# Optimization experiments

Measured on AMD Instinct MI355X. Metric: run time of the kernel, lower is better.

Reference implementation:

```python
import jax, jax.numpy as jnp
import numpy as np

B, S = 512, 200            # batch, max_seq_len
D = H = 512                # embedding_dim must equal hidden_dim (ht init from embedded input)
VOCAB, USERS, SKILLS, OUT = 2002, 10000, 1001, 1001


def setup_inputs() -> dict:
    key = jax.random.key(0)
    ks = jax.random.split(key, 15)
    s = 0.05
    enc_emb = jax.random.normal(ks[0], (VOCAB, D)) * s
    enc_emb = enc_emb.at[0].set(0.0)  # padding_idx=0
    P = jax.random.normal(ks[1], (USERS, H)) * s
    Q = jax.random.normal(ks[2], (SKILLS, H)) * s
    P_bias = jax.random.normal(ks[3], (USERS, 1)) * s
    Q_bias = jax.random.normal(ks[4], (SKILLS, 1)) * s
    W_ih = jax.random.normal(ks[5], (4 * H, D)) * s   # torch LSTMCell weight_ih
    W_hh = jax.random.normal(ks[6], (4 * H, H)) * s   # torch LSTMCell weight_hh
    b_ih = jax.random.normal(ks[7], (4 * H,)) * s
    b_hh = jax.random.normal(ks[8], (4 * H,)) * s
    dec_W = jax.random.normal(ks[9], (OUT, H)) * s    # nn.Linear weight
    dec_b = jax.random.normal(ks[10], (OUT,)) * s
    main_input = jax.random.randint(ks[11], (B, S), 0, VOCAB)
    target_id = jax.random.randint(ks[12], (B, 1), 0, OUT)
    user_id_sequence = jax.random.randint(ks[13], (B, S), 0, USERS)
    skill_id_sequence = jax.random.randint(ks[14], (B, S), 0, SKILLS)
    return dict(main_input=main_input, target_id=target_id,
                user_id_sequence=user_id_sequence, skill_id_sequence=skill_id_sequence,
                enc_emb=enc_emb, P=P, Q=Q, P_bias=P_bias, Q_bias=Q_bias,
                W_ih=W_ih, W_hh=W_hh, b_ih=b_ih, b_hh=b_hh, dec_W=dec_W, dec_b=dec_b)


def reference(main_input, target_id, user_id_sequence, skill_id_sequence,
              enc_emb, P, Q, P_bias, Q_bias, W_ih, W_hh, b_ih, b_hh, dec_W, dec_b):
    x = enc_emb[main_input]                                    # [B,S,D] (dropout in eval mode = identity)
    # MF extended input: sigmoid(sum(P*Q, dim=2, keepdim) + P_bias + Q_bias) -> [B,S,1]
    mf = jax.nn.sigmoid(jnp.sum(P[user_id_sequence] * Q[skill_id_sequence], axis=2, keepdims=True)
                        + P_bias[user_id_sequence] + Q_bias[skill_id_sequence])

    def step(carry, inp):
        ht, ct = carry
        xt, et = inp                                           # xt:[B,D], et:[B,1]
        ct = ct + ct * et                                      # custom gating before cell update
        gates = xt @ W_ih.T + b_ih + ht @ W_hh.T + b_hh        # [B,4H], torch gate order i,f,g,o
        i, f, g, o = jnp.split(gates, 4, axis=-1)
        ct = jax.nn.sigmoid(f) * ct + jax.nn.sigmoid(i) * jnp.tanh(g)
        ht = jax.nn.sigmoid(o) * jnp.tanh(ct)
        return (ht, ct), None

    h0 = jnp.zeros((x.shape[0], H), x.dtype)
    (ht, _), _ = jax.lax.scan(step, (h0, h0),
                              (jnp.swapaxes(x, 0, 1), jnp.swapaxes(mf, 0, 1)))
    out = ht @ dec_W.T + dec_b                                 # [B,OUT]
    out = jnp.take_along_axis(out, target_id, axis=-1)         # [B,1]
    return jax.nn.sigmoid(out)
```

## Files before the change

### kernel.cpp

```cpp
#include <hip/hip_runtime.h>

typedef __attribute__((ext_vector_type(8))) short short8;
typedef __attribute__((ext_vector_type(4))) float floatx4;
typedef unsigned int uint;
typedef unsigned short ushort;
typedef unsigned long long ull;

#define B_ 512
#define S_ 200
#define H_ 512
#define VOCAB_ 2002

__device__ __forceinline__ ushort f2bfbits(float f) {
  union { float f; uint u; } c; c.f = f;
  uint u = c.u;
  u += 0x7fffu + ((u >> 16) & 1u);
  return (ushort)(u >> 16);
}
__device__ __forceinline__ float bf2f_(ushort u) {
  union { uint i; float f; } c; c.i = ((uint)u) << 16; return c.f;
}
__device__ __forceinline__ float sigmoidf_(float x) { return 1.f / (1.f + __expf(-x)); }
__device__ __forceinline__ float tanhf_(float x) { return 2.f / (1.f + __expf(-2.f * x)) - 1.f; }
__device__ __forceinline__ float clamp30(float x) { return fminf(fmaxf(x, -30.f), 30.f); }

__device__ __forceinline__ void split8(const float* p, short8& hi, short8& lo) {
#pragma unroll
  for (int j = 0; j < 8; ++j) {
    const float f = p[j];
    const ushort h = f2bfbits(f);
    hi[j] = (short)h;
    lo[j] = (short)f2bfbits(f - bf2f_(h));
  }
}

template <typename ET>
__global__ void encg_kernel(const float* __restrict__ emb, const float* __restrict__ Wih,
                            ET* __restrict__ encg) {
  const int w = threadIdx.x >> 6, l = threadIdx.x & 63;
  const int ln = l & 15, lk = l >> 4;
  const int n = (blockIdx.x * 4 + w) * 16 + ln;
  const int m = blockIdx.y * 16 + ln;
  const int mA = (m < VOCAB_) ? m : 0;
  const float* ap = emb + (size_t)mA * 512 + lk * 8;
  const float* bp = Wih + (size_t)n * 512 + lk * 8;
  floatx4 acc = {0.f, 0.f, 0.f, 0.f};
#pragma unroll 4
  for (int kk = 0; kk < 16; ++kk) {
    short8 ah, al, bh, bl;
    split8(ap + kk * 32, ah, al);
    split8(bp + kk * 32, bh, bl);
    acc = __builtin_amdgcn_mfma_f32_16x16x32_bf16(ah, bh, acc, 0, 0, 0);
    acc = __builtin_amdgcn_mfma_f32_16x16x32_bf16(ah, bl, acc, 0, 0, 0);
    acc = __builtin_amdgcn_mfma_f32_16x16x32_bf16(al, bh, acc, 0, 0, 0);
  }
#pragma unroll
  for (int r = 0; r < 4; ++r) {
    const int mo = blockIdx.y * 16 + lk * 4 + r;
    if (mo < VOCAB_) {
      if constexpr (sizeof(ET) == 2)
        encg[(size_t)mo * 2048 + n] = (ET)f2bfbits(acc[r]);
      else
        encg[(size_t)mo * 2048 + n] = acc[r];
    }
  }
}

__global__ void mf_kernel(const int* __restrict__ us, const int* __restrict__ ss,
                          const float* __restrict__ P, const float* __restrict__ Q,
                          const float* __restrict__ Pb, const float* __restrict__ Qb,
                          float* __restrict__ etb) {
  const int s = blockIdx.x;
  const int w = threadIdx.x >> 6, l = threadIdx.x & 63;
  const int b = blockIdx.y * 4 + w;
  const int u = us[b * S_ + s];
  const int k = ss[b * S_ + s];
  const float4 p0 = *(const float4*)(P + (size_t)u * 512 + l * 8);
  const float4 p1 = *(const float4*)(P + (size_t)u * 512 + l * 8 + 4);
  const float4 q0 = *(const float4*)(Q + (size_t)k * 512 + l * 8);
  const float4 q1 = *(const float4*)(Q + (size_t)k * 512 + l * 8 + 4);
  float dot = p0.x*q0.x + p0.y*q0.y + p0.z*q0.z + p0.w*q0.w
            + p1.x*q1.x + p1.y*q1.y + p1.z*q1.z + p1.w*q1.w;
#pragma unroll
  for (int off = 32; off > 0; off >>= 1) dot += __shfl_xor(dot, off);
  if (l == 0)
    etb[s * B_ + b] = sigmoidf_(dot + Pb[u] + Qb[k]);
}

template <typename ET>
__global__ __launch_bounds__(512, 2) void lstm_kernel(
    const int* __restrict__ tok, const ET* __restrict__ encg,
    const float* __restrict__ etb, const float* __restrict__ Whh,
    const float* __restrict__ bih, const float* __restrict__ bhh,
    ushort* ht_hi, ushort* ht_lo, int* ctr) {
  __shared__ __align__(16) ushort Ah_lds[32 * 528];
  __shared__ __align__(16) ushort Al_lds[32 * 528];
  __shared__ __align__(16) float gp_lds[128 * 36];

  const int bid = blockIdx.x;
  const int g = bid & 15, ns = bid >> 4;
  const int b0 = g * 32, h0 = ns * 32;
  const int tid = threadIdx.x;
  const int w = tid >> 6, l = tid & 63;
  const int ln = l & 15, lk = l >> 4;
  const int q = w >> 1;
  const int c0 = (w & 1) * 16;

  int* const myslot = ctr + g * 256 + ns * 16;
  int* const gslots = ctr + g * 256;

  short8 Bh[16], Bl[16];
  {
    const float* wr = Whh + (size_t)(q * 512 + h0 + c0 + ln) * 512 + lk * 8;
#pragma unroll 4
    for (int kk = 0; kk < 16; ++kk)
      split8(wr + kk * 32, Bh[kk], Bl[kk]);
  }

  const int sr = tid >> 4;
  const int sc = tid & 15;
  const int hh = sc * 2;
  const int bg = b0 + sr;
  float ct0 = 0.f, ct1 = 0.f;

  float bs[4][2];
#pragma unroll
  for (int qq = 0; qq < 4; ++qq) {
    const int col = qq * 512 + h0 + hh;
    bs[qq][0] = bih[col] + bhh[col];
    bs[qq][1] = bih[col + 1] + bhh[col + 1];
  }

  for (int s = 0; s < S_; ++s) {
    const int tv = tok[bg * S_ + s];
    float ev = etb[s * B_ + bg];
    float ex[4], ey[4];
#pragma unroll
    for (int qq = 0; qq < 4; ++qq) {
      if constexpr (sizeof(ET) == 2) {
        const uint e2 = *(const uint*)((const ushort*)encg + (size_t)tv * 2048 + qq * 512 + h0 + hh);
        ex[qq] = bf2f_((ushort)(e2 & 0xffffu)); ey[qq] = bf2f_((ushort)(e2 >> 16));
      } else {
        const float2 e = *(const float2*)((const float*)encg + (size_t)tv * 2048 + qq * 512 + h0 + hh);
        ex[qq] = e.x; ey[qq] = e.y;
      }
    }

    if (s > 0) {
      if (tid < 16) {
        while (__hip_atomic_load(gslots + tid * 16, __ATOMIC_RELAXED,
                                 __HIP_MEMORY_SCOPE_AGENT) < s) {}
      }
      __syncthreads();
    }
    const size_t rdo = (size_t)(s & 1) * (B_ * H_);
    const size_t wro = (size_t)((s & 1) ^ 1) * (B_ * H_);

    {
      const size_t go = rdo + (size_t)(b0 + sr) * 512 + sc * 32;
      const int lo_ = sr * 528 + sc * 32;
#pragma unroll
      for (int i = 0; i < 8; ++i)
        *(ull*)(Ah_lds + lo_ + i * 4) =
            __hip_atomic_load((const ull*)(ht_hi + go + i * 4), __ATOMIC_RELAXED, __HIP_MEMORY_SCOPE_AGENT);
#pragma unroll
      for (int i = 0; i < 8; ++i)
        *(ull*)(Al_lds + lo_ + i * 4) =
            __hip_atomic_load((const ull*)(ht_lo + go + i * 4), __ATOMIC_RELAXED, __HIP_MEMORY_SCOPE_AGENT);
    }
    __syncthreads();

    floatx4 acc[2];
    acc[0] = (floatx4){0.f, 0.f, 0.f, 0.f};
    acc[1] = (floatx4){0.f, 0.f, 0.f, 0.f};
#pragma unroll
    for (int mt = 0; mt < 2; ++mt)
#pragma unroll
      for (int kk = 0; kk < 16; ++kk) {
        const int ao = (mt * 16 + ln) * 528 + kk * 32 + lk * 8;
        const short8 ah = *(const short8*)(Ah_lds + ao);
        const short8 al = *(const short8*)(Al_lds + ao);
        acc[mt] = __builtin_amdgcn_mfma_f32_16x16x32_bf16(ah, Bh[kk], acc[mt], 0, 0, 0);
        acc[mt] = __builtin_amdgcn_mfma_f32_16x16x32_bf16(ah, Bl[kk], acc[mt], 0, 0, 0);
        acc[mt] = __builtin_amdgcn_mfma_f32_16x16x32_bf16(al, Bh[kk], acc[mt], 0, 0, 0);
      }
#pragma unroll
    for (int mt = 0; mt < 2; ++mt)
      *(floatx4*)(gp_lds + (w * 16 + ln) * 36 + mt * 16 + lk * 4) = acc[mt];
    __syncthreads();

    {
      ev = fminf(fmaxf(ev, 0.f), 1.f);
      float Gv[4][2];
#pragma unroll
      for (int qq = 0; qq < 4; ++qq) {
        Gv[qq][0] = clamp30(gp_lds[(qq * 32 + hh) * 36 + sr] + ex[qq] + bs[qq][0]);
        Gv[qq][1] = clamp30(gp_lds[(qq * 32 + hh + 1) * 36 + sr] + ey[qq] + bs[qq][1]);
      }
      const float scale = 1.f + ev;
      float c0v = ct0 * scale;
      c0v = sigmoidf_(Gv[1][0]) * c0v + sigmoidf_(Gv[0][0]) * tanhf_(Gv[2][0]);
      const float h0v = sigmoidf_(Gv[3][0]) * tanhf_(c0v);
      ct0 = c0v;
      float c1v = ct1 * scale;
      c1v = sigmoidf_(Gv[1][1]) * c1v + sigmoidf_(Gv[0][1]) * tanhf_(Gv[2][1]);
      const float h1v = sigmoidf_(Gv[3][1]) * tanhf_(c1v);
      ct1 = c1v;
      const ushort h0h = f2bfbits(h0v), h1h = f2bfbits(h1v);
      const ushort h0l = f2bfbits(h0v - bf2f_(h0h)), h1l = f2bfbits(h1v - bf2f_(h1h));
      const size_t wo = wro + (size_t)bg * 512 + h0 + hh;
      __hip_atomic_store((uint*)(ht_hi + wo), (uint)h0h | ((uint)h1h << 16),
                         __ATOMIC_RELAXED, __HIP_MEMORY_SCOPE_AGENT);
      __hip_atomic_store((uint*)(ht_lo + wo), (uint)h0l | ((uint)h1l << 16),
                         __ATOMIC_RELAXED, __HIP_MEMORY_SCOPE_AGENT);
    }
    __syncthreads();
    if (tid == 0)
      __hip_atomic_store(myslot, s + 1, __ATOMIC_RELAXED, __HIP_MEMORY_SCOPE_AGENT);
  }
}

__global__ void dec_kernel(const ushort* __restrict__ hthi, const ushort* __restrict__ htlo,
                           const float* __restrict__ decW, const float* __restrict__ decb,
                           const int* __restrict__ tgt, float* __restrict__ out) {
  const int w = threadIdx.x >> 6, l = threadIdx.x & 63;
  const int b = blockIdx.x * 4 + w;
  const int t = tgt[b];
  const uint4 hv = *(const uint4*)(hthi + (size_t)b * 512 + l * 8);
  const uint4 lv = *(const uint4*)(htlo + (size_t)b * 512 + l * 8);
  const float4 w0 = *(const float4*)(decW + (size_t)t * 512 + l * 8);
  const float4 w1 = *(const float4*)(decW + (size_t)t * 512 + l * 8 + 4);
  const uint ha[4] = {hv.x, hv.y, hv.z, hv.w};
  const uint la[4] = {lv.x, lv.y, lv.z, lv.w};
  float hf[8];
#pragma unroll
  for (int i = 0; i < 4; ++i) {
    hf[2*i]   = bf2f_((ushort)(ha[i] & 0xffffu)) + bf2f_((ushort)(la[i] & 0xffffu));
    hf[2*i+1] = bf2f_((ushort)(ha[i] >> 16))     + bf2f_((ushort)(la[i] >> 16));
  }
  float dot = hf[0]*w0.x + hf[1]*w0.y + hf[2]*w0.z + hf[3]*w0.w
            + hf[4]*w1.x + hf[5]*w1.y + hf[6]*w1.z + hf[7]*w1.w;
#pragma unroll
  for (int off = 32; off > 0; off >>= 1) dot += __shfl_xor(dot, off);
  if (l == 0) out[b] = sigmoidf_(dot + decb[t]);
}

extern "C" void kernel_launch(void* const* d_in, const int* in_sizes, int n_in,
                              void* d_out, int out_size, void* d_ws, size_t ws_size,
                              hipStream_t stream) {
  (void)in_sizes; (void)n_in; (void)out_size;
  const int* main_input = (const int*)d_in[0];
  const int* target_id  = (const int*)d_in[1];
  const int* user_seq   = (const int*)d_in[2];
  const int* skill_seq  = (const int*)d_in[3];
  const float* enc_emb  = (const float*)d_in[4];
  const float* P        = (const float*)d_in[5];
  const float* Q        = (const float*)d_in[6];
  const float* Pb       = (const float*)d_in[7];
  const float* Qb       = (const float*)d_in[8];
  const float* W_ih     = (const float*)d_in[9];
  const float* W_hh     = (const float*)d_in[10];
  const float* b_ih     = (const float*)d_in[11];
  const float* b_hh     = (const float*)d_in[12];
  const float* dec_W    = (const float*)d_in[13];
  const float* dec_b    = (const float*)d_in[14];
  float* out = (float*)d_out;

  char* wsb = (char*)d_ws;
  ushort* ht_hi = (ushort*)wsb;
  ushort* ht_lo = (ushort*)(wsb + 1048576);
  int* ctr = (int*)(wsb + 2097152);
  float* etb = (float*)(wsb + 2113536);
  char* encb = wsb + 2523136;
  const bool enc32 = ws_size >= (size_t)2523136 + 16400384;

  hipMemsetAsync(wsb, 0, 2113536, stream);

  if (enc32)
    encg_kernel<float><<<dim3(32, 126), dim3(256), 0, stream>>>(enc_emb, W_ih, (float*)encb);
  else
    encg_kernel<ushort><<<dim3(32, 126), dim3(256), 0, stream>>>(enc_emb, W_ih, (ushort*)encb);
  mf_kernel<<<dim3(200, 128), dim3(256), 0, stream>>>(user_seq, skill_seq, P, Q, Pb, Qb, etb);
  if (enc32)
    lstm_kernel<float><<<dim3(256), dim3(512), 0, stream>>>(
        main_input, (const float*)encb, etb, W_hh, b_ih, b_hh, ht_hi, ht_lo, ctr);
  else
    lstm_kernel<ushort><<<dim3(256), dim3(512), 0, stream>>>(
        main_input, (const ushort*)encb, etb, W_hh, b_ih, b_hh, ht_hi, ht_lo, ctr);
  dec_kernel<<<dim3(128), dim3(256), 0, stream>>>(ht_hi, ht_lo, dec_W, dec_b, target_id, out);
}
```

Before: 2.988 ms.

## Per-wave completion flags, split h-load pipelining, and XOR-swizzled LDS in LSTM step

Each wave now publishes its own progress flag after waiting on its stores, so the end-of-step block barrier goes away. Pollers read 8 wave flags per block with coherent (sc0 sc1) vector loads. The previous hidden state is loaded in two halves, and the second half is fetched while the MFMAs on the first half run. The LDS padding is replaced by an XOR swizzle, and the gate-staging stride becomes 37. This targets per-step sync and load latency in the serial recurrence, at the cost of hand-written inline asm and more flag polling traffic.

```diff
diff --git a/kernel.cpp b/kernel.cpp
--- a/kernel.cpp
+++ b/kernel.cpp
@@ -5,6 +5,8 @@
 typedef unsigned int uint;
 typedef unsigned short ushort;
 typedef unsigned long long ull;
+typedef __attribute__((ext_vector_type(4))) uint uintx4;
+typedef __attribute__((ext_vector_type(4))) int intx4;
 
 #define B_ 512
 #define S_ 200
@@ -32,6 +34,24 @@
     hi[j] = (short)h;
     lo[j] = (short)f2bfbits(f - bf2f_(h));
   }
+}
+
+__device__ __forceinline__ void ld32_cc(const void* p, uintx4& a, uintx4& b) {
+  asm volatile("global_load_dwordx4 %0, %2, off sc0 sc1\n\t"
+               "global_load_dwordx4 %1, %2, off offset:16 sc0 sc1"
+               : "=&v"(a), "=&v"(b)
+               : "v"(p));
+}
+__device__ __forceinline__ void ld32_cc_wait(const void* p, intx4& a, intx4& b) {
+  asm volatile("global_load_dwordx4 %0, %2, off sc0 sc1\n\t"
+               "global_load_dwordx4 %1, %2, off offset:16 sc0 sc1\n\t"
+               "s_waitcnt vmcnt(0)"
+               : "=&v"(a), "=&v"(b)
+               : "v"(p)
+               : "memory");
+}
+__device__ __forceinline__ void vm_wait0() {
+  asm volatile("s_waitcnt vmcnt(0)" ::: "memory");
 }
 
 template <typename ET>
@@ -93,9 +113,9 @@
     const float* __restrict__ etb, const float* __restrict__ Whh,
     const float* __restrict__ bih, const float* __restrict__ bhh,
     ushort* ht_hi, ushort* ht_lo, int* ctr) {
-  __shared__ __align__(16) ushort Ah_lds[32 * 528];
-  __shared__ __align__(16) ushort Al_lds[32 * 528];
-  __shared__ __align__(16) float gp_lds[128 * 36];
+  __shared__ __align__(16) ushort Ah_lds[32 * 512];
+  __shared__ __align__(16) ushort Al_lds[32 * 512];
+  __shared__ float gp_lds[128 * 37];
 
   const int bid = blockIdx.x;
   const int g = bid & 15, ns = bid >> 4;
@@ -104,14 +124,14 @@
   const int w = tid >> 6, l = tid & 63;
   const int ln = l & 15, lk = l >> 4;
   const int q = w >> 1;
-  const int c0 = (w & 1) * 16;
+  const int c0w = (w & 1) * 16;
 
   int* const myslot = ctr + g * 256 + ns * 16;
-  int* const gslots = ctr + g * 256;
+  const int* const gslots = ctr + g * 256;
 
   short8 Bh[16], Bl[16];
   {
-    const float* wr = Whh + (size_t)(q * 512 + h0 + c0 + ln) * 512 + lk * 8;
+    const float* wr = Whh + (size_t)(q * 512 + h0 + c0w + ln) * 512 + lk * 8;
 #pragma unroll 4
     for (int kk = 0; kk < 16; ++kk)
       split8(wr + kk * 32, Bh[kk], Bl[kk]);
@@ -130,6 +150,9 @@
     bs[qq][0] = bih[col] + bhh[col];
     bs[qq][1] = bih[col + 1] + bhh[col + 1];
   }
+
+  const int swzw = (sr & 7) << 3;
+  const int swzr = (ln & 7) << 3;
 
   for (int s = 0; s < S_; ++s) {
     const int tv = tok[bg * S_ + s];
@@ -146,47 +169,102 @@
       }
     }
 
-    if (s > 0) {
-      if (tid < 16) {
-        while (__hip_atomic_load(gslots + tid * 16, __ATOMIC_RELAXED,
-                                 __HIP_MEMORY_SCOPE_AGENT) < s) {}
-      }
-      __syncthreads();
-    }
+    if (s > 0 && tid < 16) {
+      const int* sp = gslots + tid * 16;
+      for (;;) {
+        intx4 va, vb;
+        ld32_cc_wait(sp, va, vb);
+        if (va[0] >= s && va[1] >= s && va[2] >= s && va[3] >= s &&
+            vb[0] >= s && vb[1] >= s && vb[2] >= s && vb[3] >= s) break;
+      }
+    }
+    __syncthreads();
+
     const size_t rdo = (size_t)(s & 1) * (B_ * H_);
     const size_t wro = (size_t)((s & 1) ^ 1) * (B_ * H_);
+    const ushort* hrow = ht_hi + rdo + (size_t)bg * 512;
+    const ushort* lrow = ht_lo + rdo + (size_t)bg * 512;
 
     {
-      const size_t go = rdo + (size_t)(b0 + sr) * 512 + sc * 32;
-      const int lo_ = sr * 528 + sc * 32;
-#pragma unroll
-      for (int i = 0; i < 8; ++i)
-        *(ull*)(Ah_lds + lo_ + i * 4) =
-            __hip_atomic_load((const ull*)(ht_hi + go + i * 4), __ATOMIC_RELAXED, __HIP_MEMORY_SCOPE_AGENT);
-#pragma unroll
-      for (int i = 0; i < 8; ++i)
-        *(ull*)(Al_lds + lo_ + i * 4) =
-            __hip_atomic_load((const ull*)(ht_lo + go + i * 4), __ATOMIC_RELAXED, __HIP_MEMORY_SCOPE_AGENT);
+      const int c = sc * 16;
+      uintx4 ah0, ah1, al0, al1;
+      ld32_cc(hrow + c, ah0, ah1);
+      ld32_cc(lrow + c, al0, al1);
+      vm_wait0();
+      const int d0 = sr * 512 + (c ^ swzw);
+      const int d1 = sr * 512 + ((c + 8) ^ swzw);
+      *(uintx4*)(Ah_lds + d0) = ah0; *(uintx4*)(Ah_lds + d1) = ah1;
+      *(uintx4*)(Al_lds + d0) = al0; *(uintx4*)(Al_lds + d1) = al1;
     }
     __syncthreads();
 
-    floatx4 acc[2];
-    acc[0] = (floatx4){0.f, 0.f, 0.f, 0.f};
-    acc[1] = (floatx4){0.f, 0.f, 0.f, 0.f};
-#pragma unroll
-    for (int mt = 0; mt < 2; ++mt)
-#pragma unroll
-      for (int kk = 0; kk < 16; ++kk) {
-        const int ao = (mt * 16 + ln) * 528 + kk * 32 + lk * 8;
+    const int c1 = 256 + sc * 16;
+    uintx4 nh0, nh1, nl0, nl1;
+    ld32_cc(hrow + c1, nh0, nh1);
+    ld32_cc(lrow + c1, nl0, nl1);
+
+    floatx4 acc0 = {0.f, 0.f, 0.f, 0.f};
+    floatx4 acc1 = {0.f, 0.f, 0.f, 0.f};
+#pragma unroll
+    for (int kk = 0; kk < 8; ++kk) {
+      const int csw = (kk * 32 + lk * 8) ^ swzr;
+      {
+        const int ao = ln * 512 + csw;
         const short8 ah = *(const short8*)(Ah_lds + ao);
         const short8 al = *(const short8*)(Al_lds + ao);
-        acc[mt] = __builtin_amdgcn_mfma_f32_16x16x32_bf16(ah, Bh[kk], acc[mt], 0, 0, 0);
-        acc[mt] = __builtin_amdgcn_mfma_f32_16x16x32_bf16(ah, Bl[kk], acc[mt], 0, 0, 0);
-        acc[mt] = __builtin_amdgcn_mfma_f32_16x16x32_bf16(al, Bh[kk], acc[mt], 0, 0, 0);
-      }
-#pragma unroll
-    for (int mt = 0; mt < 2; ++mt)
-      *(floatx4*)(gp_lds + (w * 16 + ln) * 36 + mt * 16 + lk * 4) = acc[mt];
+        acc0 = __builtin_amdgcn_mfma_f32_16x16x32_bf16(ah, Bh[kk], acc0, 0, 0, 0);
+        acc0 = __builtin_amdgcn_mfma_f32_16x16x32_bf16(ah, Bl[kk], acc0, 0, 0, 0);
+        acc0 = __builtin_amdgcn_mfma_f32_16x16x32_bf16(al, Bh[kk], acc0, 0, 0, 0);
+      }
+      {
+        const int ao = (16 + ln) * 512 + csw;
+        const short8 ah = *(const short8*)(Ah_lds + ao);
+        const short8 al = *(const short8*)(Al_lds + ao);
+        acc1 = __builtin_amdgcn_mfma_f32_16x16x32_bf16(ah, Bh[kk], acc1, 0, 0, 0);
+        acc1 = __builtin_amdgcn_mfma_f32_16x16x32_bf16(ah, Bl[kk], acc1, 0, 0, 0);
+        acc1 = __builtin_amdgcn_mfma_f32_16x16x32_bf16(al, Bh[kk], acc1, 0, 0, 0);
+      }
+    }
+
+    vm_wait0();
+    __builtin_amdgcn_sched_barrier(0);
+    {
+      const int d0 = sr * 512 + (c1 ^ swzw);
+      const int d1 = sr * 512 + ((c1 + 8) ^ swzw);
+      *(uintx4*)(Ah_lds + d0) = nh0; *(uintx4*)(Ah_lds + d1) = nh1;
+      *(uintx4*)(Al_lds + d0) = nl0; *(uintx4*)(Al_lds + d1) = nl1;
+    }
+    __syncthreads();
+
+#pragma unroll
+    for (int kk = 8; kk < 16; ++kk) {
+      const int csw = (kk * 32 + lk * 8) ^ swzr;
+      {
+        const int ao = ln * 512 + csw;
+        const short8 ah = *(const short8*)(Ah_lds + ao);
+        const short8 al = *(const short8*)(Al_lds + ao);
+        acc0 = __builtin_amdgcn_mfma_f32_16x16x32_bf16(ah, Bh[kk], acc0, 0, 0, 0);
+        acc0 = __builtin_amdgcn_mfma_f32_16x16x32_bf16(ah, Bl[kk], acc0, 0, 0, 0);
+        acc0 = __builtin_amdgcn_mfma_f32_16x16x32_bf16(al, Bh[kk], acc0, 0, 0, 0);
+      }
+      {
+        const int ao = (16 + ln) * 512 + csw;
+        const short8 ah = *(const short8*)(Ah_lds + ao);
+        const short8 al = *(const short8*)(Al_lds + ao);
+        acc1 = __builtin_amdgcn_mfma_f32_16x16x32_bf16(ah, Bh[kk], acc1, 0, 0, 0);
+        acc1 = __builtin_amdgcn_mfma_f32_16x16x32_bf16(ah, Bl[kk], acc1, 0, 0, 0);
+        acc1 = __builtin_amdgcn_mfma_f32_16x16x32_bf16(al, Bh[kk], acc1, 0, 0, 0);
+      }
+    }
+
+    {
+      const int gb = (w * 16 + ln) * 37;
+#pragma unroll
+      for (int r = 0; r < 4; ++r) {
+        gp_lds[gb + lk * 4 + r] = acc0[r];
+        gp_lds[gb + 16 + lk * 4 + r] = acc1[r];
+      }
+    }
     __syncthreads();
 
     {
@@ -194,8 +272,8 @@
       float Gv[4][2];
 #pragma unroll
       for (int qq = 0; qq < 4; ++qq) {
-        Gv[qq][0] = clamp30(gp_lds[(qq * 32 + hh) * 36 + sr] + ex[qq] + bs[qq][0]);
-        Gv[qq][1] = clamp30(gp_lds[(qq * 32 + hh + 1) * 36 + sr] + ey[qq] + bs[qq][1]);
+        Gv[qq][0] = clamp30(gp_lds[(qq * 32 + hh) * 37 + sr] + ex[qq] + bs[qq][0]);
+        Gv[qq][1] = clamp30(gp_lds[(qq * 32 + hh + 1) * 37 + sr] + ey[qq] + bs[qq][1]);
       }
       const float scale = 1.f + ev;
       float c0v = ct0 * scale;
@@ -214,9 +292,10 @@
       __hip_atomic_store((uint*)(ht_lo + wo), (uint)h0l | ((uint)h1l << 16),
                          __ATOMIC_RELAXED, __HIP_MEMORY_SCOPE_AGENT);
     }
-    __syncthreads();
-    if (tid == 0)
-      __hip_atomic_store(myslot, s + 1, __ATOMIC_RELAXED, __HIP_MEMORY_SCOPE_AGENT);
+
+    vm_wait0();
+    if (l == 0)
+      __hip_atomic_store(myslot + w, s + 1, __ATOMIC_RELAXED, __HIP_MEMORY_SCOPE_AGENT);
   }
 }
 
```

Result: faster. 2.871 ms (-3.9%).
